# Performance work log

Measured on AMD Instinct MI355X. Metric: run time of the kernel, lower is better.

Reference implementation:

```python
import jax, jax.numpy as jnp
import numpy as np

N, E = 50000, 400000
F, P = 20, 8          # NUM_FREQ, NUM_POWER_CLASS (edge/node attn dim)
D, H = 128, 8         # d_model, heads
C = D // H            # head dim
FF, L = 512, 2        # dim_feedforward, num layers
EPS = 1e-5


def setup_inputs() -> dict:
    key = jax.random.key(0)
    ks = jax.random.split(key, 24)
    g = lambda k, s: jax.random.normal(k, s, dtype=jnp.float32) * 0.02
    return {
        "freq_alloc": jax.random.normal(ks[0], (N, F), jnp.float32),
        "node_power_attn": jax.random.normal(ks[1], (N, P), jnp.float32),
        "edge_power_attn": jax.random.normal(ks[2], (E, P), jnp.float32),
        "edge_index": jax.random.randint(ks[3], (2, E), 0, N),
        "ptr": jnp.sort(jax.random.randint(ks[4], (65,), 0, N)),
        # GraphTransformer input/embedding projections
        "W_in": g(ks[5], (F, D)), "b_in": jnp.zeros((D,), jnp.float32),
        "W_emb": g(ks[6], (P, D)), "b_emb": jnp.zeros((D,), jnp.float32),
        # per-layer TransformerConv params (stacked over L)
        "Wq": g(ks[7], (L, D, D)), "bq": jnp.zeros((L, D), jnp.float32),
        "Wk": g(ks[8], (L, D, D)), "bk": jnp.zeros((L, D), jnp.float32),
        "Wv": g(ks[9], (L, D, D)), "bv": jnp.zeros((L, D), jnp.float32),
        "We": g(ks[10], (L, P, D)),                      # lin_edge, bias=False
        "Wskip": g(ks[11], (L, D, D)), "bskip": jnp.zeros((L, D), jnp.float32),
        # per-layer FFN + LayerNorms
        "W1": g(ks[12], (L, D, FF)), "b1": jnp.zeros((L, FF), jnp.float32),
        "W2": g(ks[13], (L, FF, D)), "b2": jnp.zeros((L, D), jnp.float32),
        "ln1_g": jnp.ones((L, D), jnp.float32), "ln1_b": jnp.zeros((L, D), jnp.float32),
        "ln2_g": jnp.ones((L, D), jnp.float32), "ln2_b": jnp.zeros((L, D), jnp.float32),
        # output head
        "W_out": g(ks[14], (D, F)), "b_out": jnp.zeros((F,), jnp.float32),
    }


def _ln(x, g, b):
    mu = jnp.mean(x, axis=-1, keepdims=True)
    var = jnp.mean(jnp.square(x - mu), axis=-1, keepdims=True)
    return (x - mu) * jax.lax.rsqrt(var + EPS) * g + b


def reference(freq_alloc, node_power_attn, edge_power_attn, edge_index, ptr,
              W_in, b_in, W_emb, b_emb,
              Wq, bq, Wk, bk, Wv, bv, We, Wskip, bskip,
              W1, b1, W2, b2, ln1_g, ln1_b, ln2_g, ln2_b,
              W_out, b_out):
    # dropout layers are identity (inference / dropout=0)
    src, dst = edge_index[0], edge_index[1]  # PyG: messages flow src -> dst
    inp = freq_alloc @ W_in + b_in           # [N, D]
    x = node_power_attn @ W_emb + b_emb      # [N, D]
    scale = jnp.float32(1.0 / np.sqrt(C))
    for l in range(L):
        x = x + inp
        # --- TransformerConv (heads concat, root_weight=True, beta=False) ---
        q = (x @ Wq[l] + bq[l]).reshape(N, H, C)
        k = (x @ Wk[l] + bk[l]).reshape(N, H, C)
        v = (x @ Wv[l] + bv[l]).reshape(N, H, C)
        e = (edge_power_attn @ We[l]).reshape(E, H, C)   # edge embedding
        kj = k[src] + e                                   # [E, H, C]
        alpha = jnp.einsum('ehc,ehc->eh', q[dst], kj) * scale  # [E, H]
        # segment softmax over incoming edges of each dst node
        m = jnp.full((N, H), -jnp.inf, alpha.dtype).at[dst].max(alpha)
        ex = jnp.exp(alpha - m[dst])
        s = jnp.zeros((N, H), alpha.dtype).at[dst].add(ex)
        a = ex / s[dst]                                   # [E, H]
        msg = (v[src] + e) * a[:, :, None]                # [E, H, C]
        agg = jnp.zeros((N, H, C), x.dtype).at[dst].add(msg).reshape(N, D)
        x2 = agg + x @ Wskip[l] + bskip[l]
        # --- residual + norm + FFN + norm ---
        x = _ln(x + x2, ln1_g[l], ln1_b[l])
        x2 = jax.nn.relu(x @ W1[l] + b1[l]) @ W2[l] + b2[l]
        x = _ln(x + x2, ln2_g[l], ln2_b[l])
    logit = x @ W_out + b_out                             # [N, F]
    unallocated = jnp.sum(freq_alloc, axis=1, keepdims=True) < 1.0
    return jnp.where(unallocated, logit, -jnp.inf)
```

## Files before the change

### kernel.cpp

```cpp
#include <hip/hip_runtime.h>
#include <cstdint>
#include <cstddef>

typedef unsigned int uint;
typedef unsigned short ushort;
typedef __attribute__((ext_vector_type(8))) short bf16x8;
typedef __attribute__((ext_vector_type(8))) ushort u16x8;
typedef __attribute__((ext_vector_type(4))) float f32x4;
typedef __attribute__((ext_vector_type(2))) _Float16 h2v;

__device__ __forceinline__ ushort f2bf(float x) {
    uint u = __float_as_uint(x);
    u += 0x7fffu + ((u >> 16) & 1u);
    return (ushort)(u >> 16);
}
__device__ __forceinline__ float bflo(uint w) { return __uint_as_float(w << 16); }
__device__ __forceinline__ float bfhi(uint w) { return __uint_as_float(w & 0xffff0000u); }
__device__ __forceinline__ float bf1(ushort u) { return __uint_as_float(((uint)u) << 16); }
__device__ __forceinline__ uint pack2(float a, float b) { return (uint)f2bf(a) | ((uint)f2bf(b) << 16); }
__device__ __forceinline__ uint pack2h(float a, float b) {
    union { _Float16 h[2]; uint u; } c;
    c.h[0] = (_Float16)a; c.h[1] = (_Float16)b; return c.u;
}
__device__ __forceinline__ h2v ash2(uint u) { union { uint u; h2v h; } c; c.u = u; return c.h; }
__device__ __forceinline__ float dot2f(uint a, uint b, float c) {
#if __has_builtin(__builtin_amdgcn_fdot2)
    return __builtin_amdgcn_fdot2(ash2(a), ash2(b), c, false);
#else
    h2v x = ash2(a), y = ash2(b);
    return c + (float)x[0] * (float)y[0] + (float)x[1] * (float)y[1];
#endif
}


__global__ __launch_bounds__(256) void k_zero_i(int* __restrict__ p, int n) {
    int i = blockIdx.x * 256 + threadIdx.x;
    if (i < n) p[i] = 0;
}

__global__ __launch_bounds__(256) void k_count(const int* __restrict__ dst, int* __restrict__ cnt, int n) {
    int i = blockIdx.x * 256 + threadIdx.x;
    if (i < n) atomicAdd(&cnt[dst[i]], 1);
}

__global__ __launch_bounds__(256) void k_scan1(const int* __restrict__ cnt, int* __restrict__ tmp,
                                               int* __restrict__ bsums, int n) {
    __shared__ int sc[256];
    int t = threadIdx.x;
    int base = blockIdx.x * 1024 + t * 4;
    int v0 = (base + 0 < n) ? cnt[base + 0] : 0;
    int v1 = (base + 1 < n) ? cnt[base + 1] : 0;
    int v2 = (base + 2 < n) ? cnt[base + 2] : 0;
    int v3 = (base + 3 < n) ? cnt[base + 3] : 0;
    int s = v0 + v1 + v2 + v3;
    sc[t] = s;
    __syncthreads();
    for (int off = 1; off < 256; off <<= 1) {
        int u = (t >= off) ? sc[t - off] : 0;
        __syncthreads();
        sc[t] += u;
        __syncthreads();
    }
    int excl = sc[t] - s;
    int r0 = excl + v0, r1 = r0 + v1, r2 = r1 + v2, r3 = r2 + v3;
    if (base + 0 < n) tmp[base + 0] = r0;
    if (base + 1 < n) tmp[base + 1] = r1;
    if (base + 2 < n) tmp[base + 2] = r2;
    if (base + 3 < n) tmp[base + 3] = r3;
    if (t == 255) bsums[blockIdx.x] = sc[255];
}

__global__ void k_scan2(int* __restrict__ bsums, int nb) {
    int l = threadIdx.x;
    int v = (l < nb) ? bsums[l] : 0;
    int incl = v;
    for (int off = 1; off < 64; off <<= 1) {
        int u = __shfl_up(incl, off);
        if (l >= off) incl += u;
    }
    if (l < nb) bsums[l] = incl - v;
}

__global__ __launch_bounds__(256) void k_scan3(const int* __restrict__ tmp, const int* __restrict__ bsums,
                                               int* __restrict__ rowptr, int n) {
    int t = threadIdx.x;
    int base = blockIdx.x * 1024 + t * 4;
    int off = bsums[blockIdx.x];
    #pragma unroll
    for (int i = 0; i < 4; i++) {
        int g = base + i;
        if (g < n) rowptr[g + 1] = tmp[g] + off;
    }
    if (blockIdx.x == 0 && t == 0) rowptr[0] = 0;
}

__global__ __launch_bounds__(256) void k_fill(
    const int* __restrict__ src, const int* __restrict__ dst,
    const int* __restrict__ rowptr, int* __restrict__ cur,
    const float* __restrict__ epa,
    int* __restrict__ srcp, ushort* __restrict__ epap, int n) {
    int e = blockIdx.x * 256 + threadIdx.x;
    if (e < n) {
        int d = dst[e];
        int pos = atomicAdd(&cur[d], 1);
        int slot = rowptr[d] + pos;
        srcp[slot] = src[e];
        float4 a = *(const float4*)(epa + (size_t)e * 8);
        float4 b = *(const float4*)(epa + (size_t)e * 8 + 4);
        u16x8 u;
        u[0] = f2bf(a.x); u[1] = f2bf(a.y); u[2] = f2bf(a.z); u[3] = f2bf(a.w);
        u[4] = f2bf(b.x); u[5] = f2bf(b.y); u[6] = f2bf(b.z); u[7] = f2bf(b.w);
        *(u16x8*)(epap + (size_t)slot * 8) = u;
    }
}

__global__ __launch_bounds__(256) void k_prep(
    const float* __restrict__ Wq, const float* __restrict__ Wk,
    const float* __restrict__ Wv, const float* __restrict__ Ws,
    const float* __restrict__ W1, const float* __restrict__ W2,
    ushort* __restrict__ qkvsT, ushort* __restrict__ W1T, ushort* __restrict__ W2T) {
    int tid = blockIdx.x * 256 + threadIdx.x;
    int l = tid / 196608;
    int r = tid % 196608;
    if (r < 65536) {
        int which = r >> 14, e = r & 16383;
        int k = e >> 7, c = e & 127;
        const float* s = (which == 0) ? Wq : (which == 1) ? Wk : (which == 2) ? Wv : Ws;
        qkvsT[(size_t)l * 81920 + (which * 128 + c) * 128 + k] = f2bf(s[l * 16384 + e]);
    } else if (r < 131072) {
        int e = r - 65536;
        int k = e >> 9, c = e & 511;
        W1T[l * 65536 + c * 128 + k] = f2bf(W1[l * 65536 + e]);
    } else {
        int e = r - 131072;
        int k = e >> 7, c = e & 127;
        W2T[l * 65536 + c * 512 + k] = f2bf(W2[l * 65536 + e]);
    }
}

__global__ __launch_bounds__(256) void k_prepqe(
    const float* __restrict__ Wq, const float* __restrict__ We, const float* __restrict__ bq,
    ushort* __restrict__ qkvsT, float* __restrict__ bqe) {
    int tid = blockIdx.x * 256 + threadIdx.x;
    int l = tid / 16512, r = tid % 16512;
    if (l > 1) return;
    ushort* base = qkvsT + (size_t)l * 81920;
    if (r < 8192) {
        int hp = r >> 7, i = r & 127;
        int h = hp >> 3, p = hp & 7;
        const float* wq = Wq + (size_t)l * 16384 + i * 128 + h * 16;
        const float* we = We + (size_t)l * 1024 + p * 128 + h * 16;
        float acc = 0.f;
        #pragma unroll
        for (int c = 0; c < 16; c++) acc += wq[c] * we[c];
        base[(512 + hp) * 128 + i] = f2bf(acc);
    } else if (r < 16384) {
        int z = r - 8192;
        base[(576 + (z >> 7)) * 128 + (z & 127)] = 0;
    } else {
        int j = r - 16384;
        float v = 0.f;
        if (j < 64) {
            int h = j >> 3, p = j & 7;
            #pragma unroll
            for (int c = 0; c < 16; c++)
                v += bq[l * 128 + h * 16 + c] * We[(size_t)l * 1024 + p * 128 + h * 16 + c];
        }
        bqe[l * 128 + j] = v;
    }
}

__global__ __launch_bounds__(256) void k_prepa(
    const float* __restrict__ fa, const float* __restrict__ npa,
    ushort* __restrict__ Ab, int n) {
    int tid = blockIdx.x * 256 + threadIdx.x;
    int node = tid >> 5, j = tid & 31;
    if (node >= n) return;
    float v;
    if (j < 20)      v = fa[(size_t)node * 20 + j];
    else if (j < 28) v = npa[(size_t)node * 8 + (j - 20)];
    else             v = (j == 28) ? 1.0f : 0.f;
    Ab[tid] = f2bf(v);
}

__global__ __launch_bounds__(256) void k_prepw(
    const float* __restrict__ Win, const float* __restrict__ bin,
    const float* __restrict__ Wemb, const float* __restrict__ bemb,
    ushort* __restrict__ BtIO) {
    int tid = blockIdx.x * 256 + threadIdx.x;
    if (tid >= 8192) return;
    int col = tid >> 5, k = tid & 31;
    int c = col & 127;
    float v = 0.f;
    if (k < 20) v = Win[k * 128 + c];
    else if (col >= 128 && k < 28) v = Wemb[(k - 20) * 128 + c];
    else if (k == 28) v = (col < 128) ? bin[c] : (bin[c] + bemb[c]);
    BtIO[tid] = f2bf(v);
}

__global__ __launch_bounds__(256) void k_inproj2(
    const ushort* __restrict__ Ab, const ushort* __restrict__ Bt,
    ushort* __restrict__ inpb, ushort* __restrict__ xib, int M) {
    __shared__ char As[8192];
    __shared__ char Bs[16384];
    int t = threadIdx.x, lane = t & 63, w = t >> 6;
    int wr = w >> 1, wc = w & 1;
    int l15 = lane & 15, l4 = lane >> 4;
    int rbase = blockIdx.x * 128;

    #pragma unroll
    for (int p = 0; p < 2; p++) {
        int idx = p * 256 + t;
        int row = idx >> 2, c8 = idx & 3;
        int grow = rbase + row;
        uint4 v = make_uint4(0u, 0u, 0u, 0u);
        if (grow < M) v = *(const uint4*)(Ab + (size_t)grow * 32 + c8 * 8);
        *(uint4*)(As + ((row * 64 + c8 * 16) ^ ((row & 7) << 4))) = v;
    }
    #pragma unroll
    for (int p = 0; p < 4; p++) {
        int idx = p * 256 + t;
        int col = idx >> 2, c8 = idx & 3;
        uint4 v = *(const uint4*)(Bt + (size_t)col * 32 + c8 * 8);
        *(uint4*)(Bs + ((col * 64 + c8 * 16) ^ ((col & 7) << 4))) = v;
    }
    __syncthreads();

    bf16x8 a[4], b[8];
    #pragma unroll
    for (int m = 0; m < 4; m++) {
        int row = wr * 64 + m * 16 + l15;
        a[m] = *(const bf16x8*)(As + ((row * 64 + l4 * 16) ^ ((row & 7) << 4)));
    }
    #pragma unroll
    for (int nn = 0; nn < 8; nn++) {
        int col = wc * 128 + nn * 16 + l15;
        b[nn] = *(const bf16x8*)(Bs + ((col * 64 + l4 * 16) ^ ((col & 7) << 4)));
    }
    f32x4 acc[4][8] = {};
    #pragma unroll
    for (int m = 0; m < 4; m++)
        #pragma unroll
        for (int nn = 0; nn < 8; nn++)
            acc[m][nn] = __builtin_amdgcn_mfma_f32_16x16x32_bf16(b[nn], a[m], acc[m][nn], 0, 0, 0);

    ushort* outp = wc ? xib : inpb;
    #pragma unroll
    for (int nn = 0; nn < 8; nn++) {
        int c0 = nn * 16 + l4 * 4;
        #pragma unroll
        for (int m = 0; m < 4; m++) {
            int grow = rbase + wr * 64 + m * 16 + l15;
            if (grow >= M) continue;
            uint2 pk = make_uint2(pack2(acc[m][nn][0], acc[m][nn][1]),
                                  pack2(acc[m][nn][2], acc[m][nn][3]));
            *(uint2*)(outp + (size_t)grow * 128 + c0) = pk;
        }
    }
}

struct OutDesc5 {
    ushort* bptr[5];
    const float* bias[5];
    int bld[5];
    int wid[5];
    const ushort* res;
    int resbx;
    int f16mask;
};

__global__ __launch_bounds__(256) void k_qkvs_gemm(
    const ushort* __restrict__ A,
    const ushort* __restrict__ Bt,
    OutDesc5 od, int M) {
    __shared__ char smem[32768];
    char* As = smem;
    char* Bs = smem + 16384;
    int t = threadIdx.x;
    int lane = t & 63, w = t >> 6;
    int wr = w >> 1, wc = w & 1;
    int l15 = lane & 15, l4 = lane >> 4;
    int rbase = blockIdx.y * 128;
    int cbase = blockIdx.x * 128;
    int bx = blockIdx.x;

    f32x4 acc[4][4] = {};

    for (int kb = 0; kb < 128; kb += 64) {
        #pragma unroll
        for (int p = 0; p < 4; p++) {
            int idx = p * 256 + t;
            int row = idx >> 3, c8 = idx & 7;
            int grow = rbase + row;
            uint4 v = make_uint4(0u, 0u, 0u, 0u);
            if (grow < M) v = *(const uint4*)(A + (size_t)grow * 128 + kb + c8 * 8);
            *(uint4*)(As + ((row * 128 + c8 * 16) ^ ((row & 7) << 4))) = v;
        }
        #pragma unroll
        for (int p = 0; p < 4; p++) {
            int idx = p * 256 + t;
            int col = idx >> 3, c8 = idx & 7;
            uint4 v = *(const uint4*)(Bt + (size_t)(cbase + col) * 128 + kb + c8 * 8);
            *(uint4*)(Bs + ((col * 128 + c8 * 16) ^ ((col & 7) << 4))) = v;
        }
        __syncthreads();
        #pragma unroll
        for (int kk = 0; kk < 2; kk++) {
            int kbyte = kk * 64 + l4 * 16;
            bf16x8 a[4], b[4];
            #pragma unroll
            for (int m = 0; m < 4; m++) {
                int row = wr * 64 + m * 16 + l15;
                a[m] = *(const bf16x8*)(As + ((row * 128 + kbyte) ^ ((row & 7) << 4)));
            }
            #pragma unroll
            for (int nn = 0; nn < 4; nn++) {
                int col = wc * 64 + nn * 16 + l15;
                b[nn] = *(const bf16x8*)(Bs + ((col * 128 + kbyte) ^ ((col & 7) << 4)));
            }
            #pragma unroll
            for (int m = 0; m < 4; m++)
                #pragma unroll
                for (int nn = 0; nn < 4; nn++)
                    acc[m][nn] = __builtin_amdgcn_mfma_f32_16x16x32_bf16(b[nn], a[m], acc[m][nn], 0, 0, 0);
        }
        __syncthreads();
    }

    int wid = od.wid[bx];
    const float* bias = od.bias[bx];
    ushort* outp = od.bptr[bx];
    int bld = od.bld[bx];
    bool addres = (bx == od.resbx);
    bool f16o = (od.f16mask >> bx) & 1;
    #pragma unroll
    for (int nn = 0; nn < 4; nn++) {
        int c0 = wc * 64 + nn * 16 + l4 * 4;
        if (c0 >= wid) continue;
        float4 b4 = *(const float4*)(bias + c0);
        #pragma unroll
        for (int m = 0; m < 4; m++) {
            int grow = rbase + wr * 64 + m * 16 + l15;
            if (grow >= M) continue;
            float v0 = acc[m][nn][0] + b4.x;
            float v1 = acc[m][nn][1] + b4.y;
            float v2 = acc[m][nn][2] + b4.z;
            float v3 = acc[m][nn][3] + b4.w;
            if (addres) {
                uint2 rv = *(const uint2*)(od.res + (size_t)grow * 128 + c0);
                v0 += bflo(rv.x); v1 += bfhi(rv.x);
                v2 += bflo(rv.y); v3 += bfhi(rv.y);
            }
            uint2 pk;
            if (f16o) pk = make_uint2(pack2h(v0, v1), pack2h(v2, v3));
            else      pk = make_uint2(pack2(v0, v1), pack2(v2, v3));
            *(uint2*)(outp + (size_t)grow * bld + c0) = pk;
        }
    }
}

template <bool ADDINP>
__global__ __launch_bounds__(256) void k_ffn(
    const ushort* __restrict__ h1b,
    const ushort* __restrict__ W1T,
    const ushort* __restrict__ W2T,
    const float* __restrict__ b1, const float* __restrict__ b2,
    const float* __restrict__ g, const float* __restrict__ bb,
    const ushort* __restrict__ inpb,
    ushort* __restrict__ xib, int M) {
    __shared__ char As[16384];
    __shared__ char Wsb[16384];
    __shared__ char Hs[64 * 144];
    int t = threadIdx.x, lane = t & 63, w = t >> 6;
    int rbase = blockIdx.x * 64;
    int l15 = lane & 15, l4 = lane >> 4;

    #pragma unroll
    for (int p = 0; p < 4; p++) {
        int idx = p * 256 + t;
        int row = idx >> 4, c8 = idx & 15;
        int grow = rbase + row;
        uint4 v = make_uint4(0u, 0u, 0u, 0u);
        if (grow < M) v = *(const uint4*)(h1b + (size_t)grow * 128 + c8 * 8);
        *(uint4*)(As + ((row * 256 + c8 * 16) ^ ((row & 7) << 4))) = v;
    }

    const ushort* w1base = W1T + (size_t)(w * 16 + l15) * 128;
    bf16x8 wfn[4];
    #pragma unroll
    for (int kk = 0; kk < 4; kk++)
        wfn[kk] = *(const bf16x8*)(w1base + kk * 32 + l4 * 8);

    f32x4 acco[8] = {};
    __syncthreads();

    for (int ch = 0; ch < 8; ch++) {
        uint4 w2r[4];
        #pragma unroll
        for (int p = 0; p < 4; p++) {
            int idx = p * 256 + t;
            int oc = idx >> 3, c8 = idx & 7;
            w2r[p] = *(const uint4*)(W2T + (size_t)oc * 512 + ch * 64 + c8 * 8);
        }
        bf16x8 wfc[4];
        #pragma unroll
        for (int kk = 0; kk < 4; kk++) wfc[kk] = wfn[kk];
        if (ch < 7) {
            const ushort* nb = w1base + (size_t)(ch + 1) * 8192;
            #pragma unroll
            for (int kk = 0; kk < 4; kk++)
                wfn[kk] = *(const bf16x8*)(nb + kk * 32 + l4 * 8);
        }
        f32x4 acch[4] = {};
        #pragma unroll
        for (int kk = 0; kk < 4; kk++) {
            int kbyte = kk * 64 + l4 * 16;
            #pragma unroll
            for (int j = 0; j < 4; j++) {
                int row = j * 16 + l15;
                bf16x8 hf = *(const bf16x8*)(As + ((row * 256 + kbyte) ^ ((row & 7) << 4)));
                acch[j] = __builtin_amdgcn_mfma_f32_16x16x32_bf16(wfc[kk], hf, acch[j], 0, 0, 0);
            }
        }
        {
            int hc0 = w * 16 + l4 * 4;
            float4 b1v = *(const float4*)(b1 + ch * 64 + hc0);
            #pragma unroll
            for (int j = 0; j < 4; j++) {
                int row = j * 16 + l15;
                float v0 = fmaxf(acch[j][0] + b1v.x, 0.f);
                float v1 = fmaxf(acch[j][1] + b1v.y, 0.f);
                float v2 = fmaxf(acch[j][2] + b1v.z, 0.f);
                float v3 = fmaxf(acch[j][3] + b1v.w, 0.f);
                uint2 pk = make_uint2(pack2(v0, v1), pack2(v2, v3));
                *(uint2*)(Hs + row * 144 + hc0 * 2) = pk;
            }
        }
        #pragma unroll
        for (int p = 0; p < 4; p++) {
            int idx = p * 256 + t;
            int oc = idx >> 3, c8 = idx & 7;
            *(uint4*)(Wsb + ((oc * 128 + c8 * 16) ^ ((oc & 7) << 4))) = w2r[p];
        }
        __syncthreads();
        #pragma unroll
        for (int kk = 0; kk < 2; kk++) {
            int kbyte = kk * 64 + l4 * 16;
            bf16x8 a = *(const bf16x8*)(Hs + (w * 16 + l15) * 144 + kbyte);
            #pragma unroll
            for (int nn = 0; nn < 8; nn++) {
                int oc = nn * 16 + l15;
                bf16x8 b = *(const bf16x8*)(Wsb + ((oc * 128 + kbyte) ^ ((oc & 7) << 4)));
                acco[nn] = __builtin_amdgcn_mfma_f32_16x16x32_bf16(a, b, acco[nn], 0, 0, 0);
            }
        }
        __syncthreads();
    }

    float b2v[8], gg[8], bbv[8];
    #pragma unroll
    for (int nn = 0; nn < 8; nn++) {
        int coll = nn * 16 + l15;
        b2v[nn] = b2[coll]; gg[nn] = g[coll]; bbv[nn] = bb[coll];
    }
    #pragma unroll
    for (int r = 0; r < 4; r++) {
        int rowt = w * 16 + l4 * 4 + r;
        int grow = rbase + rowt;
        float pre[8];
        float s1 = 0.f, s2 = 0.f;
        #pragma unroll
        for (int nn = 0; nn < 8; nn++) {
            int coll = nn * 16 + l15;
            float rv = bf1(*(const ushort*)(As + ((rowt * 256 + coll * 2) ^ ((rowt & 7) << 4))));
            float v = acco[nn][r] + b2v[nn] + rv;
            pre[nn] = v;
            s1 += v; s2 += v * v;
        }
        #pragma unroll
        for (int mask = 1; mask <= 8; mask <<= 1) {
            s1 += __shfl_xor(s1, mask);
            s2 += __shfl_xor(s2, mask);
        }
        float mu = s1 * (1.f / 128.f);
        float var = s2 * (1.f / 128.f) - mu * mu;
        float rsq = rsqrtf(var + 1e-5f);
        if (grow < M) {
            #pragma unroll
            for (int nn = 0; nn < 8; nn++) {
                int coll = nn * 16 + l15;
                float v = (pre[nn] - mu) * rsq * gg[nn] + bbv[nn];
                if (ADDINP) v += bf1(inpb[(size_t)grow * 128 + coll]);
                xib[(size_t)grow * 128 + coll] = f2bf(v);
            }
        }
    }
}

__global__ __launch_bounds__(256) void k_attn(
    const ushort* __restrict__ qsb, const ushort* __restrict__ kvb,
    const ushort* __restrict__ qeb,
    const int* __restrict__ srcp, const ushort* __restrict__ epap,
    const int* __restrict__ rowptr,
    const float* __restrict__ We,
    const float* __restrict__ g1, const float* __restrict__ be1,
    ushort* __restrict__ h1, int n) {
    int wave = threadIdx.x >> 6, lane = threadIdx.x & 63;
    int nhalf = lane >> 5, l32 = lane & 31;
    int s = l32 >> 3, h = l32 & 7;
    int node = blockIdx.x * 8 + wave * 2 + nhalf;
    if (node >= n) node = n - 1;
    int d0 = h * 16 + s * 4;
    const ushort* qrow = qsb + (size_t)node * 256;
    uint4 qh0 = *(const uint4*)(qrow + h * 16);
    uint4 qh1 = *(const uint4*)(qrow + h * 16 + 8);
    uint2 sw = *(const uint2*)(qrow + 128 + d0);
    uint4 qe = *(const uint4*)(qeb + (size_t)node * 64 + h * 8);
    int beg = rowptr[node];
    int end = rowptr[node + 1];
    float4 gv = *(const float4*)(g1 + d0);
    float4 bv = *(const float4*)(be1 + d0);

    float qe8[8];
    qe8[0] = bflo(qe.x); qe8[1] = bfhi(qe.x); qe8[2] = bflo(qe.y); qe8[3] = bfhi(qe.y);
    qe8[4] = bflo(qe.z); qe8[5] = bfhi(qe.z); qe8[6] = bflo(qe.w); qe8[7] = bfhi(qe.w);

    float sacc = 0.f, va[16], awp[8];
    #pragma unroll
    for (int c = 0; c < 16; c++) va[c] = 0.f;
    #pragma unroll
    for (int p = 0; p < 8; p++) awp[p] = 0.f;

    for (int base = beg; base < end; base += 4) {
        int i = base + s;
        bool ve = i < end;
        int ii = ve ? i : beg;
        int sn = srcp[ii];
        uint4 ew = *(const uint4*)(epap + (size_t)ii * 8);
        const ushort* kr = kvb + (size_t)sn * 256 + h * 16;
        uint4 k0 = *(const uint4*)(kr);
        uint4 k1 = *(const uint4*)(kr + 8);
        uint4 v0 = *(const uint4*)(kr + 128);
        uint4 v1 = *(const uint4*)(kr + 136);
        float ep[8];
        ep[0] = bflo(ew.x); ep[1] = bfhi(ew.x); ep[2] = bflo(ew.y); ep[3] = bfhi(ew.y);
        ep[4] = bflo(ew.z); ep[5] = bfhi(ew.z); ep[6] = bflo(ew.w); ep[7] = bfhi(ew.w);
        float dt = 0.f;
        dt = dot2f(k0.x, qh0.x, dt); dt = dot2f(k0.y, qh0.y, dt);
        dt = dot2f(k0.z, qh0.z, dt); dt = dot2f(k0.w, qh0.w, dt);
        dt = dot2f(k1.x, qh1.x, dt); dt = dot2f(k1.y, qh1.y, dt);
        dt = dot2f(k1.z, qh1.z, dt); dt = dot2f(k1.w, qh1.w, dt);
        #pragma unroll
        for (int p = 0; p < 8; p++) dt += qe8[p] * ep[p];
        float ex = ve ? __expf(dt * 0.25f) : 0.f;
        sacc += ex;
        float vf[16];
        vf[0] = bflo(v0.x); vf[1] = bfhi(v0.x); vf[2] = bflo(v0.y); vf[3] = bfhi(v0.y);
        vf[4] = bflo(v0.z); vf[5] = bfhi(v0.z); vf[6] = bflo(v0.w); vf[7] = bfhi(v0.w);
        vf[8] = bflo(v1.x); vf[9] = bfhi(v1.x); vf[10] = bflo(v1.y); vf[11] = bfhi(v1.y);
        vf[12] = bflo(v1.z); vf[13] = bfhi(v1.z); vf[14] = bflo(v1.w); vf[15] = bfhi(v1.w);
        #pragma unroll
        for (int c = 0; c < 16; c++) va[c] += ex * vf[c];
        #pragma unroll
        for (int p = 0; p < 8; p++) awp[p] += ex * ep[p];
    }

    float v8[8];
    bool hiA = (s & 2) != 0;
    #pragma unroll
    for (int j = 0; j < 8; j++) {
        float keep = hiA ? va[8 + j] : va[j];
        float send = hiA ? va[j] : va[8 + j];
        v8[j] = keep + __shfl_xor(send, 16);
    }
    float v4[4];
    bool hiB = (s & 1) != 0;
    #pragma unroll
    for (int j = 0; j < 4; j++) {
        float keep = hiB ? v8[4 + j] : v8[j];
        float send = hiB ? v8[j] : v8[4 + j];
        v4[j] = keep + __shfl_xor(send, 8);
    }
    #pragma unroll
    for (int mask = 8; mask <= 16; mask <<= 1) {
        sacc += __shfl_xor(sacc, mask);
        #pragma unroll
        for (int p = 0; p < 8; p++) awp[p] += __shfl_xor(awp[p], mask);
    }

    float agg[4];
    #pragma unroll
    for (int j = 0; j < 4; j++) {
        float a = v4[j];
        #pragma unroll
        for (int p = 0; p < 8; p++) a += awp[p] * We[p * 128 + d0 + j];
        agg[j] = a;
    }
    float invs = (end > beg) ? 1.f / sacc : 0.f;

    float pre[4];
    pre[0] = agg[0] * invs + bflo(sw.x);
    pre[1] = agg[1] * invs + bfhi(sw.x);
    pre[2] = agg[2] * invs + bflo(sw.y);
    pre[3] = agg[3] * invs + bfhi(sw.y);
    float s1 = pre[0] + pre[1] + pre[2] + pre[3];
    float s2 = pre[0] * pre[0] + pre[1] * pre[1] + pre[2] * pre[2] + pre[3] * pre[3];
    #pragma unroll
    for (int off = 1; off <= 16; off <<= 1) {
        s1 += __shfl_xor(s1, off);
        s2 += __shfl_xor(s2, off);
    }
    float mu = s1 * (1.f / 128.f);
    float var = s2 * (1.f / 128.f) - mu * mu;
    float rs = rsqrtf(var + 1e-5f);
    float o0 = (pre[0] - mu) * rs * gv.x + bv.x;
    float o1 = (pre[1] - mu) * rs * gv.y + bv.y;
    float o2 = (pre[2] - mu) * rs * gv.z + bv.z;
    float o3 = (pre[3] - mu) * rs * gv.w + bv.w;
    uint2 pk = make_uint2(pack2(o0, o1), pack2(o2, o3));
    *(uint2*)(h1 + (size_t)node * 128 + d0) = pk;
}

__global__ __launch_bounds__(256) void k_out(
    const ushort* __restrict__ x, const float* __restrict__ Wout, const float* __restrict__ bout,
    const float* __restrict__ fa, float* __restrict__ out, int n) {
    __shared__ float xs[8][128];
    __shared__ float ws[128][20];
    __shared__ float bs[20];
    int t = threadIdx.x;
    int nodeBase = blockIdx.x * 8;
    for (int i = t; i < 2560; i += 256) ws[i / 20][i % 20] = Wout[i];
    if (t < 20) bs[t] = bout[t];
    {
        int row = t >> 5, c4 = t & 31;
        int node = nodeBase + row;
        int nc = node < n ? node : (n - 1);
        uint2 v = *(const uint2*)(x + (size_t)nc * 128 + c4 * 4);
        xs[row][c4 * 4 + 0] = bflo(v.x); xs[row][c4 * 4 + 1] = bfhi(v.x);
        xs[row][c4 * 4 + 2] = bflo(v.y); xs[row][c4 * 4 + 3] = bfhi(v.y);
    }
    int row = t >> 5, jj = t & 31;
    int node = nodeBase + row;
    bool vn = node < n;
    float fv = (vn && jj < 20) ? fa[(size_t)node * 20 + jj] : 0.f;
    float rsum = fv;
    #pragma unroll
    for (int m = 16; m >= 1; m >>= 1) rsum += __shfl_xor(rsum, m);
    __syncthreads();
    if (!vn || jj >= 20) return;
    float acc = bs[jj];
    #pragma unroll 16
    for (int d = 0; d < 128; d++) acc += xs[row][d] * ws[d][jj];
    out[(size_t)node * 20 + jj] = (rsum < 1.0f) ? acc : -3.0e38f;
}

extern "C" void kernel_launch(void* const* d_in, const int* in_sizes, int n_in,
                              void* d_out, int out_size, void* d_ws, size_t ws_size,
                              hipStream_t stream) {
    const float* fa    = (const float*)d_in[0];
    const float* npa   = (const float*)d_in[1];
    const float* epa   = (const float*)d_in[2];
    const int*   ei    = (const int*)d_in[3];
    const float* Win   = (const float*)d_in[5];
    const float* bin   = (const float*)d_in[6];
    const float* Wemb  = (const float*)d_in[7];
    const float* bemb  = (const float*)d_in[8];
    const float* Wq    = (const float*)d_in[9];
    const float* bqv   = (const float*)d_in[10];
    const float* Wk    = (const float*)d_in[11];
    const float* bkv   = (const float*)d_in[12];
    const float* Wv    = (const float*)d_in[13];
    const float* bvv   = (const float*)d_in[14];
    const float* We    = (const float*)d_in[15];
    const float* Wskip = (const float*)d_in[16];
    const float* bskip = (const float*)d_in[17];
    const float* W1    = (const float*)d_in[18];
    const float* b1    = (const float*)d_in[19];
    const float* W2    = (const float*)d_in[20];
    const float* b2    = (const float*)d_in[21];
    const float* ln1g  = (const float*)d_in[22];
    const float* ln1b  = (const float*)d_in[23];
    const float* ln2g  = (const float*)d_in[24];
    const float* ln2b  = (const float*)d_in[25];
    const float* Wout  = (const float*)d_in[26];
    const float* bout  = (const float*)d_in[27];

    const int N = in_sizes[0] / 20;
    const int E = in_sizes[2] / 8;

    char* wp = (char*)d_ws;
    #define WS_ALLOC(ty, name, count) ty* name = (ty*)wp; wp += (((size_t)(count) * sizeof(ty)) + 63) & ~(size_t)63;
    WS_ALLOC(ushort, xib,  (size_t)N * 128)
    WS_ALLOC(ushort, h1b,  (size_t)N * 128)
    WS_ALLOC(ushort, inpb, (size_t)N * 128)
    WS_ALLOC(ushort, qsb,  (size_t)N * 256)
    WS_ALLOC(ushort, kvb,  (size_t)N * 256)
    WS_ALLOC(ushort, qeb,  (size_t)N * 64)
    WS_ALLOC(ushort, Ab,   (size_t)N * 32)
    WS_ALLOC(ushort, qkvsT, 2 * 81920)
    WS_ALLOC(ushort, W1T,   2 * 65536)
    WS_ALLOC(ushort, W2T,   2 * 65536)
    WS_ALLOC(ushort, BtIO,  8192)
    WS_ALLOC(float,  bqe,   256)
    WS_ALLOC(ushort, epap,  (size_t)E * 8)
    WS_ALLOC(int,    srcp,  E)
    WS_ALLOC(int,    rowptr, N + 1)
    WS_ALLOC(int,    cnt,    N)
    WS_ALLOC(int,    cur,    N)
    WS_ALLOC(int,    tmp,    N)
    WS_ALLOC(int,    bsums,  64)
    #undef WS_ALLOC

    const int* srcs = ei;
    const int* dsts = ei + E;

    k_zero_i<<<(2 * N + 255) / 256, 256, 0, stream>>>(cnt, 2 * N);
    k_count<<<(E + 255) / 256, 256, 0, stream>>>(dsts, cnt, E);
    int nb = (N + 1023) / 1024;
    k_scan1<<<nb, 256, 0, stream>>>(cnt, tmp, bsums, N);
    k_scan2<<<1, 64, 0, stream>>>(bsums, nb);
    k_scan3<<<nb, 256, 0, stream>>>(tmp, bsums, rowptr, N);
    k_fill<<<(E + 255) / 256, 256, 0, stream>>>(srcs, dsts, rowptr, cur, epa, srcp, epap, E);

    k_prep<<<1536, 256, 0, stream>>>(Wq, Wk, Wv, Wskip, W1, W2, qkvsT, W1T, W2T);
    k_prepqe<<<130, 256, 0, stream>>>(Wq, We, bqv, qkvsT, bqe);
    k_prepw<<<32, 256, 0, stream>>>(Win, bin, Wemb, bemb, BtIO);
    k_prepa<<<((size_t)N * 32 + 255) / 256, 256, 0, stream>>>(fa, npa, Ab, N);

    int qblocks = (N + 127) / 128;
    int fblocks = (N + 63) / 64;

    k_inproj2<<<qblocks, 256, 0, stream>>>(Ab, BtIO, inpb, xib, N);

    for (int l = 0; l < 2; l++) {
        {
            OutDesc5 od = {};
            od.bptr[0] = qsb;        od.bias[0] = bqv + l * 128;   od.bld[0] = 256; od.wid[0] = 128;
            od.bptr[1] = kvb;        od.bias[1] = bkv + l * 128;   od.bld[1] = 256; od.wid[1] = 128;
            od.bptr[2] = kvb + 128;  od.bias[2] = bvv + l * 128;   od.bld[2] = 256; od.wid[2] = 128;
            od.bptr[3] = qsb + 128;  od.bias[3] = bskip + l * 128; od.bld[3] = 256; od.wid[3] = 128;
            od.bptr[4] = qeb;        od.bias[4] = bqe + l * 128;   od.bld[4] = 64;  od.wid[4] = 64;
            od.res = xib; od.resbx = 3;
            od.f16mask = 0b00011;
            k_qkvs_gemm<<<dim3(5, qblocks), 256, 0, stream>>>(
                xib, qkvsT + (size_t)l * 81920, od, N);
        }

        k_attn<<<(N + 7) / 8, 256, 0, stream>>>(qsb, kvb, qeb, srcp, epap, rowptr,
                                                We + (size_t)l * 1024,
                                                ln1g + l * 128, ln1b + l * 128, h1b, N);

        if (l == 0)
            k_ffn<true><<<fblocks, 256, 0, stream>>>(
                h1b, W1T, W2T, b1, b2, ln2g, ln2b, inpb, xib, N);
        else
            k_ffn<false><<<fblocks, 256, 0, stream>>>(
                h1b, W1T + 65536, W2T + 65536, b1 + 512, b2 + 128,
                ln2g + 128, ln2b + 128, nullptr, xib, N);
    }

    k_out<<<(N + 7) / 8, 256, 0, stream>>>(xib, Wout, bout, fa, (float*)d_out, N);
}
```

Baseline: 347.2 us.

## Unroll attention edge loop by two, vectorize We loads, remap GEMM blocks per XCD

The attention gather loop now handles two edges per lane each iteration, putting twice as many independent K/V/edge loads in flight to hide gather latency. The per-column We reads become float4 vector loads. The QKV GEMM switches to a 1D grid whose block IDs are remapped so consecutive logical tiles land on the same XCD, improving L2 reuse of A rows across the five column tiles. In exchange the loop uses more registers, which may lower occupancy.

```diff
diff --git a/kernel.cpp b/kernel.cpp
--- a/kernel.cpp
+++ b/kernel.cpp
@@ -280,9 +280,14 @@
     int lane = t & 63, w = t >> 6;
     int wr = w >> 1, wc = w & 1;
     int l15 = lane & 15, l4 = lane >> 4;
-    int rbase = blockIdx.y * 128;
-    int cbase = blockIdx.x * 128;
-    int bx = blockIdx.x;
+    int nwg = gridDim.x;
+    int id = blockIdx.x;
+    int q8 = nwg >> 3, r8 = nwg & 7;
+    int xcd = id & 7, pos = id >> 3;
+    int logical = (xcd < r8 ? xcd * (q8 + 1) : r8 * (q8 + 1) + (xcd - r8) * q8) + pos;
+    int bx = logical % 5;
+    int rbase = (logical / 5) * 128;
+    int cbase = bx * 128;
 
     f32x4 acc[4][4] = {};
 
@@ -531,38 +536,60 @@
     #pragma unroll
     for (int p = 0; p < 8; p++) awp[p] = 0.f;
 
-    for (int base = beg; base < end; base += 4) {
-        int i = base + s;
-        bool ve = i < end;
-        int ii = ve ? i : beg;
-        int sn = srcp[ii];
-        uint4 ew = *(const uint4*)(epap + (size_t)ii * 8);
-        const ushort* kr = kvb + (size_t)sn * 256 + h * 16;
-        uint4 k0 = *(const uint4*)(kr);
-        uint4 k1 = *(const uint4*)(kr + 8);
-        uint4 v0 = *(const uint4*)(kr + 128);
-        uint4 v1 = *(const uint4*)(kr + 136);
-        float ep[8];
-        ep[0] = bflo(ew.x); ep[1] = bfhi(ew.x); ep[2] = bflo(ew.y); ep[3] = bfhi(ew.y);
-        ep[4] = bflo(ew.z); ep[5] = bfhi(ew.z); ep[6] = bflo(ew.w); ep[7] = bfhi(ew.w);
-        float dt = 0.f;
-        dt = dot2f(k0.x, qh0.x, dt); dt = dot2f(k0.y, qh0.y, dt);
-        dt = dot2f(k0.z, qh0.z, dt); dt = dot2f(k0.w, qh0.w, dt);
-        dt = dot2f(k1.x, qh1.x, dt); dt = dot2f(k1.y, qh1.y, dt);
-        dt = dot2f(k1.z, qh1.z, dt); dt = dot2f(k1.w, qh1.w, dt);
-        #pragma unroll
-        for (int p = 0; p < 8; p++) dt += qe8[p] * ep[p];
-        float ex = ve ? __expf(dt * 0.25f) : 0.f;
-        sacc += ex;
-        float vf[16];
-        vf[0] = bflo(v0.x); vf[1] = bfhi(v0.x); vf[2] = bflo(v0.y); vf[3] = bfhi(v0.y);
-        vf[4] = bflo(v0.z); vf[5] = bfhi(v0.z); vf[6] = bflo(v0.w); vf[7] = bfhi(v0.w);
-        vf[8] = bflo(v1.x); vf[9] = bfhi(v1.x); vf[10] = bflo(v1.y); vf[11] = bfhi(v1.y);
-        vf[12] = bflo(v1.z); vf[13] = bfhi(v1.z); vf[14] = bflo(v1.w); vf[15] = bfhi(v1.w);
-        #pragma unroll
-        for (int c = 0; c < 16; c++) va[c] += ex * vf[c];
-        #pragma unroll
-        for (int p = 0; p < 8; p++) awp[p] += ex * ep[p];
+    for (int base = beg; base < end; base += 8) {
+        int iA = base + s, iB = base + 4 + s;
+        bool veA = iA < end, veB = iB < end;
+        int iiA = veA ? iA : end - 1;
+        int iiB = veB ? iB : end - 1;
+        int snA = srcp[iiA];
+        int snB = srcp[iiB];
+        uint4 ewA = *(const uint4*)(epap + (size_t)iiA * 8);
+        uint4 ewB = *(const uint4*)(epap + (size_t)iiB * 8);
+        const ushort* krA = kvb + (size_t)snA * 256 + h * 16;
+        const ushort* krB = kvb + (size_t)snB * 256 + h * 16;
+        uint4 kA0 = *(const uint4*)(krA);
+        uint4 kA1 = *(const uint4*)(krA + 8);
+        uint4 vA0 = *(const uint4*)(krA + 128);
+        uint4 vA1 = *(const uint4*)(krA + 136);
+        uint4 kB0 = *(const uint4*)(krB);
+        uint4 kB1 = *(const uint4*)(krB + 8);
+        uint4 vB0 = *(const uint4*)(krB + 128);
+        uint4 vB1 = *(const uint4*)(krB + 136);
+
+        float epA[8], epB[8];
+        epA[0] = bflo(ewA.x); epA[1] = bfhi(ewA.x); epA[2] = bflo(ewA.y); epA[3] = bfhi(ewA.y);
+        epA[4] = bflo(ewA.z); epA[5] = bfhi(ewA.z); epA[6] = bflo(ewA.w); epA[7] = bfhi(ewA.w);
+        epB[0] = bflo(ewB.x); epB[1] = bfhi(ewB.x); epB[2] = bflo(ewB.y); epB[3] = bfhi(ewB.y);
+        epB[4] = bflo(ewB.z); epB[5] = bfhi(ewB.z); epB[6] = bflo(ewB.w); epB[7] = bfhi(ewB.w);
+
+        float dtA = 0.f, dtB = 0.f;
+        dtA = dot2f(kA0.x, qh0.x, dtA); dtB = dot2f(kB0.x, qh0.x, dtB);
+        dtA = dot2f(kA0.y, qh0.y, dtA); dtB = dot2f(kB0.y, qh0.y, dtB);
+        dtA = dot2f(kA0.z, qh0.z, dtA); dtB = dot2f(kB0.z, qh0.z, dtB);
+        dtA = dot2f(kA0.w, qh0.w, dtA); dtB = dot2f(kB0.w, qh0.w, dtB);
+        dtA = dot2f(kA1.x, qh1.x, dtA); dtB = dot2f(kB1.x, qh1.x, dtB);
+        dtA = dot2f(kA1.y, qh1.y, dtA); dtB = dot2f(kB1.y, qh1.y, dtB);
+        dtA = dot2f(kA1.z, qh1.z, dtA); dtB = dot2f(kB1.z, qh1.z, dtB);
+        dtA = dot2f(kA1.w, qh1.w, dtA); dtB = dot2f(kB1.w, qh1.w, dtB);
+        #pragma unroll
+        for (int p = 0; p < 8; p++) { dtA += qe8[p] * epA[p]; dtB += qe8[p] * epB[p]; }
+        float exA = veA ? __expf(dtA * 0.25f) : 0.f;
+        float exB = veB ? __expf(dtB * 0.25f) : 0.f;
+        sacc += exA + exB;
+
+        float vfA[16], vfB[16];
+        vfA[0] = bflo(vA0.x); vfA[1] = bfhi(vA0.x); vfA[2] = bflo(vA0.y); vfA[3] = bfhi(vA0.y);
+        vfA[4] = bflo(vA0.z); vfA[5] = bfhi(vA0.z); vfA[6] = bflo(vA0.w); vfA[7] = bfhi(vA0.w);
+        vfA[8] = bflo(vA1.x); vfA[9] = bfhi(vA1.x); vfA[10] = bflo(vA1.y); vfA[11] = bfhi(vA1.y);
+        vfA[12] = bflo(vA1.z); vfA[13] = bfhi(vA1.z); vfA[14] = bflo(vA1.w); vfA[15] = bfhi(vA1.w);
+        vfB[0] = bflo(vB0.x); vfB[1] = bfhi(vB0.x); vfB[2] = bflo(vB0.y); vfB[3] = bfhi(vB0.y);
+        vfB[4] = bflo(vB0.z); vfB[5] = bfhi(vB0.z); vfB[6] = bflo(vB0.w); vfB[7] = bfhi(vB0.w);
+        vfB[8] = bflo(vB1.x); vfB[9] = bfhi(vB1.x); vfB[10] = bflo(vB1.y); vfB[11] = bfhi(vB1.y);
+        vfB[12] = bflo(vB1.z); vfB[13] = bfhi(vB1.z); vfB[14] = bflo(vB1.w); vfB[15] = bfhi(vB1.w);
+        #pragma unroll
+        for (int c = 0; c < 16; c++) va[c] += exA * vfA[c] + exB * vfB[c];
+        #pragma unroll
+        for (int p = 0; p < 8; p++) awp[p] += exA * epA[p] + exB * epB[p];
     }
 
     float v8[8];
@@ -589,12 +616,17 @@
     }
 
     float agg[4];
-    #pragma unroll
-    for (int j = 0; j < 4; j++) {
-        float a = v4[j];
-        #pragma unroll
-        for (int p = 0; p < 8; p++) a += awp[p] * We[p * 128 + d0 + j];
-        agg[j] = a;
+    {
+        float4 we4[8];
+        #pragma unroll
+        for (int p = 0; p < 8; p++) we4[p] = *(const float4*)(We + p * 128 + d0);
+        #pragma unroll
+        for (int j = 0; j < 4; j++) {
+            float a = v4[j];
+            #pragma unroll
+            for (int p = 0; p < 8; p++) a += awp[p] * ((const float*)&we4[p])[j];
+            agg[j] = a;
+        }
     }
     float invs = (end > beg) ? 1.f / sacc : 0.f;
 
@@ -742,7 +774,7 @@
             od.bptr[4] = qeb;        od.bias[4] = bqe + l * 128;   od.bld[4] = 64;  od.wid[4] = 64;
             od.res = xib; od.resbx = 3;
             od.f16mask = 0b00011;
-            k_qkvs_gemm<<<dim3(5, qblocks), 256, 0, stream>>>(
+            k_qkvs_gemm<<<5 * qblocks, 256, 0, stream>>>(
                 xib, qkvsT + (size_t)l * 81920, od, N);
         }
 
```

New measurement: 379.4 us. +9.3%, slower.
